# Performance work log

Measured on AMD Instinct MI355X. Metric: run time of the kernel, lower is better.

The kernel has to match this reference:

```python
import jax, jax.numpy as jnp
import numpy as np

N_ACTIVE = 100000
C = 64
N_BLOCKS = 2
K = 27  # 3x3x3 submanifold rulebook offsets
BN_EPS = 1e-4  # scn BatchNorm default eps


def setup_inputs() -> dict:
    key = jax.random.key(0)
    k1, k2, k3 = jax.random.split(key, 3)
    feats = jax.random.normal(k1, (N_ACTIVE, C), dtype=jnp.float32)
    # rulebook: index N_ACTIVE == missing neighbor (points at padded zero row)
    nbrs = jax.random.randint(k2, (N_ACTIVE, K), 0, N_ACTIVE + 1, dtype=jnp.int32)
    # make the center offset (k=13) point at self, as in a real submanifold rulebook
    nbrs = nbrs.at[:, K // 2].set(jnp.arange(N_ACTIVE, dtype=jnp.int32))
    fan_in = K * C
    W = jax.random.normal(k3, (N_BLOCKS, 2, K, C, C), dtype=jnp.float32) / np.sqrt(fan_in)
    gamma = jnp.ones((N_BLOCKS, 2, C), dtype=jnp.float32)
    beta = jnp.zeros((N_BLOCKS, 2, C), dtype=jnp.float32)
    return {"feats": feats, "nbrs": nbrs, "W": W, "gamma": gamma, "beta": beta}


def _subm_conv(x, nbrs, Wk):
    # x: [N, C]; nbrs: [N, K] with value N meaning 'missing'; Wk: [K, C, C]
    x_pad = jnp.concatenate([x, jnp.zeros((1, x.shape[1]), x.dtype)], axis=0)
    g = x_pad[nbrs]  # [N, K, C] rulebook gather
    return jnp.einsum('nkc,kcd->nd', g, Wk)  # gather-GEMM-scatter fused by contraction


def _bn(x, g, b):
    mu = jnp.mean(x, axis=0)
    var = jnp.var(x, axis=0)
    return (x - mu) * jax.lax.rsqrt(var + BN_EPS) * g + b


def reference(feats, nbrs, W, gamma, beta):
    x = feats
    for i in range(N_BLOCKS):  # SparseResidualBlock chain
        residual = x
        out = _subm_conv(x, nbrs, W[i, 0])
        out = jax.nn.relu(_bn(out, gamma[i, 0], beta[i, 0]))  # BatchNormReLU
        out = _subm_conv(out, nbrs, W[i, 1])
        out = _bn(out, gamma[i, 1], beta[i, 1])  # BatchNormalization
        x = jax.nn.relu(out + residual)  # AddTable + ReLU
    return x
```

## Files before the change

### kernel.cpp

```cpp
#include <hip/hip_runtime.h>

#define N_PTS 100000
#define NT_STRIDE 100096
#define NK 27
#define NKP 28
#define TOTAL (N_PTS * 64)
#define NB_CONV 1564

typedef short bf16x8 __attribute__((ext_vector_type(8)));
typedef float f32x4 __attribute__((ext_vector_type(4)));
typedef unsigned short u16x8 __attribute__((ext_vector_type(8)));

__device__ __forceinline__ unsigned short f2bf(float f) {
    unsigned u = __builtin_bit_cast(unsigned, f);
    u += 0x7fffu + ((u >> 16) & 1u);
    return (unsigned short)(u >> 16);
}
__device__ __forceinline__ float bf2f(unsigned short u) {
    return __builtin_bit_cast(float, ((unsigned)u) << 16);
}

__global__ void cast_in_k(const float* __restrict__ feats, unsigned short* __restrict__ xb) {
    int t = blockIdx.x * 256 + threadIdx.x;
    if (t >= (N_PTS + 1) * 8) return;
    int i = t * 8;
    u16x8 o;
    if (i < TOTAL) {
        f32x4 v0 = ((const f32x4*)(feats + i))[0];
        f32x4 v1 = ((const f32x4*)(feats + i))[1];
#pragma unroll
        for (int j = 0; j < 4; ++j) { o[j] = f2bf(v0[j]); o[4 + j] = f2bf(v1[j]); }
    } else {
#pragma unroll
        for (int j = 0; j < 8; ++j) o[j] = 0;
    }
    *(u16x8*)(xb + i) = o;
}

__global__ void tr_nbrs_k(const int* __restrict__ nbrs, int* __restrict__ nbrsT) {
    __shared__ int tile[64 * 28];
    const int n0 = blockIdx.x * 64;
    const int t = threadIdx.x;
    const int base = n0 * 27;
    for (int i = t; i < 1728; i += 256) {
        int v = (base + i < N_PTS * 27) ? nbrs[base + i] : N_PTS;
        int r = i / 27, c = i - r * 27;
        tile[r * 28 + c] = v;
    }
    __syncthreads();
    for (int i = t; i < 1728; i += 256) {
        int k = i >> 6, j = i & 63;
        nbrsT[(size_t)k * NT_STRIDE + n0 + j] = tile[j * 28 + k];
    }
    for (int i = t; i < 64; i += 256)
        nbrsT[(size_t)27 * NT_STRIDE + n0 + i] = N_PTS;
}

__global__ void pack_w_k(const float* __restrict__ W, unsigned short* __restrict__ Wp) {
    int o = blockIdx.x * 256 + threadIdx.x;
    if (o >= 4 * NKP * 4096) return;
    int conv = o / (NKP * 4096);
    int r = o - conv * (NKP * 4096);
    int k = r >> 12;
    if (k == 27) { Wp[o] = 0; return; }
    int r2 = r & 4095;
    int frag = r2 >> 9;
    int kk = frag >> 2, cb = frag & 3;
    int lane = (r2 >> 3) & 63;
    int j = r2 & 7;
    int c = kk * 32 + (lane >> 4) * 8 + j;
    int d = cb * 16 + (lane & 15);
    Wp[o] = f2bf(W[(size_t)(conv * NK + k) * 4096 + c * 64 + d]);
}

__global__ __launch_bounds__(256, 4) void conv_k(
    const unsigned short* __restrict__ xb,
    const int* __restrict__ nbrsT,
    const unsigned short* __restrict__ Wp,
    unsigned short* __restrict__ ybf,
    float* __restrict__ partials)
{
    const int tid = threadIdx.x;
    const int lane = tid & 63;
    const int wave = tid >> 6;
    const int l15 = lane & 15;
    const int lgrp = lane >> 4;
    const int h = wave & 1;
    const int kh = wave >> 1;
    const int wave_row = blockIdx.x * 64 + h * 32;
    const int r0 = wave_row + l15;
    const int r1 = r0 + 16;
    const int k0 = kh * 14;

    f32x4 acc[2][4];
#pragma unroll
    for (int m = 0; m < 2; ++m)
#pragma unroll
        for (int cb = 0; cb < 4; ++cb) acc[m][cb] = (f32x4)0.f;

    const bf16x8* wp = (const bf16x8*)Wp;

    int id0[4], id1[4];
#pragma unroll
    for (int s = 0; s < 4; ++s) {
        id0[s] = nbrsT[(size_t)(k0 + s) * NT_STRIDE + r0];
        id1[s] = nbrsT[(size_t)(k0 + s) * NT_STRIDE + r1];
    }
    bf16x8 apf[3][4];
#pragma unroll
    for (int s = 0; s < 2; ++s) {
        const bf16x8* p0 = (const bf16x8*)(xb + (size_t)id0[s] * 64);
        const bf16x8* p1 = (const bf16x8*)(xb + (size_t)id1[s] * 64);
        apf[s][0] = p0[lgrp]; apf[s][1] = p0[4 + lgrp];
        apf[s][2] = p1[lgrp]; apf[s][3] = p1[4 + lgrp];
    }

#pragma unroll
    for (int s = 0; s < 14; ++s) {
        if (s + 4 < 14) {
            id0[s & 3] = nbrsT[(size_t)(k0 + s + 4) * NT_STRIDE + r0];
            id1[s & 3] = nbrsT[(size_t)(k0 + s + 4) * NT_STRIDE + r1];
        }
        if (s + 2 < 14) {
            const int j = (s + 2) & 3;
            const int st = (s + 2) % 3;
            const bf16x8* p0 = (const bf16x8*)(xb + (size_t)id0[j] * 64);
            const bf16x8* p1 = (const bf16x8*)(xb + (size_t)id1[j] * 64);
            apf[st][0] = p0[lgrp]; apf[st][1] = p0[4 + lgrp];
            apf[st][2] = p1[lgrp]; apf[st][3] = p1[4 + lgrp];
        }
        __builtin_amdgcn_sched_barrier(0);
        const int st = s % 3;
        const bf16x8* wk = wp + (size_t)(k0 + s) * 512 + lane;
        {
            bf16x8 b0 = wk[0], b1 = wk[64], b2 = wk[128], b3 = wk[192];
            acc[0][0] = __builtin_amdgcn_mfma_f32_16x16x32_bf16(apf[st][0], b0, acc[0][0], 0, 0, 0);
            acc[1][0] = __builtin_amdgcn_mfma_f32_16x16x32_bf16(apf[st][2], b0, acc[1][0], 0, 0, 0);
            acc[0][1] = __builtin_amdgcn_mfma_f32_16x16x32_bf16(apf[st][0], b1, acc[0][1], 0, 0, 0);
            acc[1][1] = __builtin_amdgcn_mfma_f32_16x16x32_bf16(apf[st][2], b1, acc[1][1], 0, 0, 0);
            acc[0][2] = __builtin_amdgcn_mfma_f32_16x16x32_bf16(apf[st][0], b2, acc[0][2], 0, 0, 0);
            acc[1][2] = __builtin_amdgcn_mfma_f32_16x16x32_bf16(apf[st][2], b2, acc[1][2], 0, 0, 0);
            acc[0][3] = __builtin_amdgcn_mfma_f32_16x16x32_bf16(apf[st][0], b3, acc[0][3], 0, 0, 0);
            acc[1][3] = __builtin_amdgcn_mfma_f32_16x16x32_bf16(apf[st][2], b3, acc[1][3], 0, 0, 0);
        }
        {
            bf16x8 b0 = wk[256], b1 = wk[320], b2 = wk[384], b3 = wk[448];
            acc[0][0] = __builtin_amdgcn_mfma_f32_16x16x32_bf16(apf[st][1], b0, acc[0][0], 0, 0, 0);
            acc[1][0] = __builtin_amdgcn_mfma_f32_16x16x32_bf16(apf[st][3], b0, acc[1][0], 0, 0, 0);
            acc[0][1] = __builtin_amdgcn_mfma_f32_16x16x32_bf16(apf[st][1], b1, acc[0][1], 0, 0, 0);
            acc[1][1] = __builtin_amdgcn_mfma_f32_16x16x32_bf16(apf[st][3], b1, acc[1][1], 0, 0, 0);
            acc[0][2] = __builtin_amdgcn_mfma_f32_16x16x32_bf16(apf[st][1], b2, acc[0][2], 0, 0, 0);
            acc[1][2] = __builtin_amdgcn_mfma_f32_16x16x32_bf16(apf[st][3], b2, acc[1][2], 0, 0, 0);
            acc[0][3] = __builtin_amdgcn_mfma_f32_16x16x32_bf16(apf[st][1], b3, acc[0][3], 0, 0, 0);
            acc[1][3] = __builtin_amdgcn_mfma_f32_16x16x32_bf16(apf[st][3], b3, acc[1][3], 0, 0, 0);
        }
    }

    __shared__ __align__(16) float ytile[64 * 68];
    __shared__ __align__(16) float sred[4][128];

    if (kh == 0) {
#pragma unroll
        for (int m = 0; m < 2; ++m)
#pragma unroll
            for (int cb = 0; cb < 4; ++cb)
#pragma unroll
                for (int r = 0; r < 4; ++r)
                    ytile[(h * 32 + m * 16 + lgrp * 4 + r) * 68 + cb * 16 + l15] = acc[m][cb][r];
    }
    __syncthreads();
    if (kh == 1) {
#pragma unroll
        for (int m = 0; m < 2; ++m)
#pragma unroll
            for (int cb = 0; cb < 4; ++cb)
#pragma unroll
                for (int r = 0; r < 4; ++r)
                    ytile[(h * 32 + m * 16 + lgrp * 4 + r) * 68 + cb * 16 + l15] += acc[m][cb][r];
    }
    __syncthreads();

    const int row = tid >> 2;
    const int colb = (tid & 3) * 16;
    f32x4 v[4];
#pragma unroll
    for (int j = 0; j < 4; ++j) v[j] = *(const f32x4*)&ytile[row * 68 + colb + 4 * j];

    const int grow = blockIdx.x * 64 + row;
    if (grow < N_PTS) {
        u16x8 o0, o1;
#pragma unroll
        for (int j = 0; j < 4; ++j) { o0[j] = f2bf(v[0][j]); o0[4 + j] = f2bf(v[1][j]); }
#pragma unroll
        for (int j = 0; j < 4; ++j) { o1[j] = f2bf(v[2][j]); o1[4 + j] = f2bf(v[3][j]); }
        *(u16x8*)(ybf + (size_t)grow * 64 + colb) = o0;
        *(u16x8*)(ybf + (size_t)grow * 64 + colb + 8) = o1;
    }

    f32x4 sv[4], s2v[4];
#pragma unroll
    for (int j = 0; j < 4; ++j) { sv[j] = v[j]; s2v[j] = v[j] * v[j]; }
#pragma unroll
    for (int off = 4; off < 64; off <<= 1) {
#pragma unroll
        for (int j = 0; j < 4; ++j) {
#pragma unroll
            for (int e = 0; e < 4; ++e) {
                sv[j][e]  += __shfl_xor(sv[j][e],  off);
                s2v[j][e] += __shfl_xor(s2v[j][e], off);
            }
        }
    }
    if (lane < 4) {
#pragma unroll
        for (int j = 0; j < 4; ++j) {
            *(f32x4*)&sred[wave][lane * 16 + 4 * j]      = sv[j];
            *(f32x4*)&sred[wave][64 + lane * 16 + 4 * j] = s2v[j];
        }
    }
    __syncthreads();
    if (tid < 128) {
        float p = sred[0][tid] + sred[1][tid] + sred[2][tid] + sred[3][tid];
        partials[(size_t)blockIdx.x * 128 + tid] = p;
    }
}

__global__ void bn_fin_k(const float* __restrict__ partials,
                         const float* __restrict__ gamma,
                         const float* __restrict__ beta,
                         float* __restrict__ scsh) {
    const int c = blockIdx.x;
    const int t = threadIdx.x;
    float s = 0.f, s2 = 0.f;
    for (int w = t; w < NB_CONV; w += 256) {
        s  += partials[(size_t)w * 128 + c];
        s2 += partials[(size_t)w * 128 + 64 + c];
    }
#pragma unroll
    for (int off = 1; off < 64; off <<= 1) {
        s  += __shfl_xor(s, off, 64);
        s2 += __shfl_xor(s2, off, 64);
    }
    __shared__ float sm[8];
    int wv = t >> 6;
    if ((t & 63) == 0) { sm[wv] = s; sm[4 + wv] = s2; }
    __syncthreads();
    if (t == 0) {
        float S  = sm[0] + sm[1] + sm[2] + sm[3];
        float S2 = sm[4] + sm[5] + sm[6] + sm[7];
        const float invN = 1.0f / (float)N_PTS;
        float mu = S * invN;
        float var = S2 * invN - mu * mu;
        float sc = gamma[c] * rsqrtf(var + 1e-4f);
        scsh[c] = sc;
        scsh[64 + c] = beta[c] - mu * sc;
    }
}

__global__ void bn_relu_cast_k(const unsigned short* __restrict__ ybf, const float* __restrict__ scsh,
                               unsigned short* __restrict__ xb) {
    int t = blockIdx.x * 256 + threadIdx.x;
    if (t >= TOTAL / 8) return;
    int i = t * 8;
    int c0 = i & 63;
    u16x8 v = *(const u16x8*)(ybf + i);
    f32x4 sa = *(const f32x4*)(scsh + c0);
    f32x4 sb = *(const f32x4*)(scsh + c0 + 4);
    f32x4 ba = *(const f32x4*)(scsh + 64 + c0);
    f32x4 bb = *(const f32x4*)(scsh + 64 + c0 + 4);
    u16x8 o;
#pragma unroll
    for (int j = 0; j < 4; ++j) {
        o[j]     = f2bf(fmaxf(bf2f(v[j])     * sa[j] + ba[j], 0.f));
        o[4 + j] = f2bf(fmaxf(bf2f(v[4 + j]) * sb[j] + bb[j], 0.f));
    }
    *(u16x8*)(xb + i) = o;
}

__global__ void bn_add_relu_k(const unsigned short* __restrict__ ybf, const float* __restrict__ scsh,
                              const float* __restrict__ res, float* __restrict__ xout,
                              unsigned short* __restrict__ xb, int writeBf) {
    int t = blockIdx.x * 256 + threadIdx.x;
    if (t >= TOTAL / 8) return;
    int i = t * 8;
    int c0 = i & 63;
    u16x8 v = *(const u16x8*)(ybf + i);
    f32x4 q0 = ((const f32x4*)(res + i))[0];
    f32x4 q1 = ((const f32x4*)(res + i))[1];
    f32x4 sa = *(const f32x4*)(scsh + c0);
    f32x4 sb = *(const f32x4*)(scsh + c0 + 4);
    f32x4 ba = *(const f32x4*)(scsh + 64 + c0);
    f32x4 bb = *(const f32x4*)(scsh + 64 + c0 + 4);
    f32x4 o0, o1;
#pragma unroll
    for (int j = 0; j < 4; ++j) {
        o0[j] = fmaxf(bf2f(v[j])     * sa[j] + ba[j] + q0[j], 0.f);
        o1[j] = fmaxf(bf2f(v[4 + j]) * sb[j] + bb[j] + q1[j], 0.f);
    }
    ((f32x4*)(xout + i))[0] = o0;
    ((f32x4*)(xout + i))[1] = o1;
    if (writeBf) {
        u16x8 o;
#pragma unroll
        for (int j = 0; j < 4; ++j) { o[j] = f2bf(o0[j]); o[4 + j] = f2bf(o1[j]); }
        *(u16x8*)(xb + i) = o;
    }
}

extern "C" void kernel_launch(void* const* d_in, const int* in_sizes, int n_in,
                              void* d_out, int out_size, void* d_ws, size_t ws_size,
                              hipStream_t stream) {
    const float* feats = (const float*)d_in[0];
    const int*   nbrs  = (const int*)d_in[1];
    const float* W     = (const float*)d_in[2];
    const float* gamma = (const float*)d_in[3];
    const float* beta  = (const float*)d_in[4];
    float* out = (float*)d_out;

    char* ws = (char*)d_ws;
    unsigned short* xb       = (unsigned short*)ws;
    unsigned short* ybf      = (unsigned short*)(ws + 12800512);
    unsigned short* Wp       = (unsigned short*)(ws + 25600512);
    int*            nbrsT    = (int*)(ws + 26518016);
    float*          partials = (float*)(ws + 37728768);
    float*          scsh     = (float*)(ws + 38529536);

    dim3 b256(256);
    cast_in_k<<<((N_PTS + 1) * 8 + 255) / 256, b256, 0, stream>>>(feats, xb);
    tr_nbrs_k<<<NT_STRIDE / 64, b256, 0, stream>>>(nbrs, nbrsT);
    pack_w_k<<<(4 * NKP * 4096) / 256, b256, 0, stream>>>(W, Wp);

    const int appl_blocks = (TOTAL / 8) / 256;
    for (int blk = 0; blk < 2; ++blk) {
        int c0 = blk * 2, c1 = blk * 2 + 1;
        conv_k<<<NB_CONV, b256, 0, stream>>>(xb, nbrsT, Wp + (size_t)c0 * NKP * 4096, ybf, partials);
        bn_fin_k<<<64, b256, 0, stream>>>(partials, gamma + c0 * 64, beta + c0 * 64, scsh);
        bn_relu_cast_k<<<appl_blocks, b256, 0, stream>>>(ybf, scsh, xb);
        conv_k<<<NB_CONV, b256, 0, stream>>>(xb, nbrsT, Wp + (size_t)c1 * NKP * 4096, ybf, partials);
        bn_fin_k<<<64, b256, 0, stream>>>(partials, gamma + c1 * 64, beta + c1 * 64, scsh);
        const float* res = (blk == 0) ? feats : (const float*)out;
        bn_add_relu_k<<<appl_blocks, b256, 0, stream>>>(ybf, scsh, res, out, xb, blk == 0 ? 1 : 0);
    }
}
```

Before: 472.8 us.

## Fuse BN+ReLU into second conv gather and use atomic BN statistics

The first BN+ReLU is now applied on the fly while the second conv gathers neighbour rows, so the separate normalize pass over the intermediate is gone. Missing neighbours are still forced to zero. The per-block partial-sum reduction kernel is replaced by atomicAdd into a small global accumulator that is zeroed once with a memset, and every consumer derives scale and shift itself. The cost is redundant BN math on each gathered row (27x per point), float-atomic contention, nondeterministic summation order, and the removal of a sched_barrier. Nontemporal loads and stores are also added.

```diff
diff --git a/kernel.cpp b/kernel.cpp
--- a/kernel.cpp
+++ b/kernel.cpp
@@ -73,12 +73,16 @@
     Wp[o] = f2bf(W[(size_t)(conv * NK + k) * 4096 + c * 64 + d]);
 }
 
+template <int FUSED>
 __global__ __launch_bounds__(256, 4) void conv_k(
-    const unsigned short* __restrict__ xb,
+    const unsigned short* __restrict__ xin,
     const int* __restrict__ nbrsT,
     const unsigned short* __restrict__ Wp,
-    unsigned short* __restrict__ ybf,
-    float* __restrict__ partials)
+    unsigned short* __restrict__ yout,
+    const float* __restrict__ gpart_in,
+    const float* __restrict__ gamma,
+    const float* __restrict__ beta,
+    float* __restrict__ gpart_out)
 {
     const int tid = threadIdx.x;
     const int lane = tid & 63;
@@ -92,6 +96,25 @@
     const int r1 = r0 + 16;
     const int k0 = kh * 14;
 
+    float sc[2][8], sh[2][8];
+    if (FUSED) {
+        const float invN = 1.0f / (float)N_PTS;
+#pragma unroll
+        for (int half = 0; half < 2; ++half) {
+            int cbase = half * 32 + lgrp * 8;
+#pragma unroll
+            for (int e = 0; e < 8; ++e) {
+                int c = cbase + e;
+                float S = gpart_in[c], S2 = gpart_in[64 + c];
+                float mu = S * invN;
+                float var = S2 * invN - mu * mu;
+                float s = gamma[c] * rsqrtf(var + 1e-4f);
+                sc[half][e] = s;
+                sh[half][e] = beta[c] - mu * s;
+            }
+        }
+    }
+
     f32x4 acc[2][4];
 #pragma unroll
     for (int m = 0; m < 2; ++m)
@@ -100,36 +123,53 @@
 
     const bf16x8* wp = (const bf16x8*)Wp;
 
+    auto ldrow = [&](int idx, bf16x8* dst) {
+        const bf16x8* p = (const bf16x8*)(xin + (size_t)idx * 64);
+        bf16x8 a0 = p[lgrp];
+        bf16x8 a1 = p[4 + lgrp];
+        if (FUSED) {
+            bool ok = (idx != N_PTS);
+            u16x8 u0 = __builtin_bit_cast(u16x8, a0);
+            u16x8 u1 = __builtin_bit_cast(u16x8, a1);
+            u16x8 o0, o1;
+#pragma unroll
+            for (int e = 0; e < 8; ++e) {
+                o0[e] = f2bf(fmaxf(bf2f(u0[e]) * sc[0][e] + sh[0][e], 0.f));
+                o1[e] = f2bf(fmaxf(bf2f(u1[e]) * sc[1][e] + sh[1][e], 0.f));
+            }
+            bf16x8 z = (bf16x8)(short)0;
+            a0 = ok ? __builtin_bit_cast(bf16x8, o0) : z;
+            a1 = ok ? __builtin_bit_cast(bf16x8, o1) : z;
+        }
+        dst[0] = a0;
+        dst[1] = a1;
+    };
+
     int id0[4], id1[4];
 #pragma unroll
     for (int s = 0; s < 4; ++s) {
-        id0[s] = nbrsT[(size_t)(k0 + s) * NT_STRIDE + r0];
-        id1[s] = nbrsT[(size_t)(k0 + s) * NT_STRIDE + r1];
+        id0[s] = __builtin_nontemporal_load(nbrsT + (size_t)(k0 + s) * NT_STRIDE + r0);
+        id1[s] = __builtin_nontemporal_load(nbrsT + (size_t)(k0 + s) * NT_STRIDE + r1);
     }
     bf16x8 apf[3][4];
 #pragma unroll
     for (int s = 0; s < 2; ++s) {
-        const bf16x8* p0 = (const bf16x8*)(xb + (size_t)id0[s] * 64);
-        const bf16x8* p1 = (const bf16x8*)(xb + (size_t)id1[s] * 64);
-        apf[s][0] = p0[lgrp]; apf[s][1] = p0[4 + lgrp];
-        apf[s][2] = p1[lgrp]; apf[s][3] = p1[4 + lgrp];
+        ldrow(id0[s], &apf[s][0]);
+        ldrow(id1[s], &apf[s][2]);
     }
 
 #pragma unroll
     for (int s = 0; s < 14; ++s) {
         if (s + 4 < 14) {
-            id0[s & 3] = nbrsT[(size_t)(k0 + s + 4) * NT_STRIDE + r0];
-            id1[s & 3] = nbrsT[(size_t)(k0 + s + 4) * NT_STRIDE + r1];
+            id0[s & 3] = __builtin_nontemporal_load(nbrsT + (size_t)(k0 + s + 4) * NT_STRIDE + r0);
+            id1[s & 3] = __builtin_nontemporal_load(nbrsT + (size_t)(k0 + s + 4) * NT_STRIDE + r1);
         }
         if (s + 2 < 14) {
             const int j = (s + 2) & 3;
-            const int st = (s + 2) % 3;
-            const bf16x8* p0 = (const bf16x8*)(xb + (size_t)id0[j] * 64);
-            const bf16x8* p1 = (const bf16x8*)(xb + (size_t)id1[j] * 64);
-            apf[st][0] = p0[lgrp]; apf[st][1] = p0[4 + lgrp];
-            apf[st][2] = p1[lgrp]; apf[st][3] = p1[4 + lgrp];
-        }
-        __builtin_amdgcn_sched_barrier(0);
+            const int st2 = (s + 2) % 3;
+            ldrow(id0[j], &apf[st2][0]);
+            ldrow(id1[j], &apf[st2][2]);
+        }
         const int st = s % 3;
         const bf16x8* wk = wp + (size_t)(k0 + s) * 512 + lane;
         {
@@ -193,8 +233,8 @@
         for (int j = 0; j < 4; ++j) { o0[j] = f2bf(v[0][j]); o0[4 + j] = f2bf(v[1][j]); }
 #pragma unroll
         for (int j = 0; j < 4; ++j) { o1[j] = f2bf(v[2][j]); o1[4 + j] = f2bf(v[3][j]); }
-        *(u16x8*)(ybf + (size_t)grow * 64 + colb) = o0;
-        *(u16x8*)(ybf + (size_t)grow * 64 + colb + 8) = o1;
+        __builtin_nontemporal_store(o0, (u16x8*)(yout + (size_t)grow * 64 + colb));
+        __builtin_nontemporal_store(o1, (u16x8*)(yout + (size_t)grow * 64 + colb + 8));
     }
 
     f32x4 sv[4], s2v[4];
@@ -221,84 +261,45 @@
     __syncthreads();
     if (tid < 128) {
         float p = sred[0][tid] + sred[1][tid] + sred[2][tid] + sred[3][tid];
-        partials[(size_t)blockIdx.x * 128 + tid] = p;
-    }
-}
-
-__global__ void bn_fin_k(const float* __restrict__ partials,
-                         const float* __restrict__ gamma,
-                         const float* __restrict__ beta,
-                         float* __restrict__ scsh) {
-    const int c = blockIdx.x;
-    const int t = threadIdx.x;
-    float s = 0.f, s2 = 0.f;
-    for (int w = t; w < NB_CONV; w += 256) {
-        s  += partials[(size_t)w * 128 + c];
-        s2 += partials[(size_t)w * 128 + 64 + c];
-    }
-#pragma unroll
-    for (int off = 1; off < 64; off <<= 1) {
-        s  += __shfl_xor(s, off, 64);
-        s2 += __shfl_xor(s2, off, 64);
-    }
-    __shared__ float sm[8];
-    int wv = t >> 6;
-    if ((t & 63) == 0) { sm[wv] = s; sm[4 + wv] = s2; }
-    __syncthreads();
-    if (t == 0) {
-        float S  = sm[0] + sm[1] + sm[2] + sm[3];
-        float S2 = sm[4] + sm[5] + sm[6] + sm[7];
-        const float invN = 1.0f / (float)N_PTS;
-        float mu = S * invN;
-        float var = S2 * invN - mu * mu;
-        float sc = gamma[c] * rsqrtf(var + 1e-4f);
-        scsh[c] = sc;
-        scsh[64 + c] = beta[c] - mu * sc;
-    }
-}
-
-__global__ void bn_relu_cast_k(const unsigned short* __restrict__ ybf, const float* __restrict__ scsh,
-                               unsigned short* __restrict__ xb) {
+        atomicAdd(&gpart_out[tid], p);
+    }
+}
+
+__global__ void bn_fuse_k(const unsigned short* __restrict__ yraw,
+                          const float* __restrict__ gpart,
+                          const float* __restrict__ gamma,
+                          const float* __restrict__ beta,
+                          const float* __restrict__ res,
+                          float* __restrict__ xout,
+                          unsigned short* __restrict__ xb, int writeBf) {
     int t = blockIdx.x * 256 + threadIdx.x;
     if (t >= TOTAL / 8) return;
     int i = t * 8;
     int c0 = i & 63;
-    u16x8 v = *(const u16x8*)(ybf + i);
-    f32x4 sa = *(const f32x4*)(scsh + c0);
-    f32x4 sb = *(const f32x4*)(scsh + c0 + 4);
-    f32x4 ba = *(const f32x4*)(scsh + 64 + c0);
-    f32x4 bb = *(const f32x4*)(scsh + 64 + c0 + 4);
-    u16x8 o;
+    u16x8 v = __builtin_nontemporal_load((const u16x8*)(yraw + i));
+    f32x4 q0 = __builtin_nontemporal_load((const f32x4*)(res + i));
+    f32x4 q1 = __builtin_nontemporal_load((const f32x4*)(res + i) + 1);
+
+    const float invN = 1.0f / (float)N_PTS;
+    float sc[8], sh[8];
+#pragma unroll
+    for (int j = 0; j < 8; ++j) {
+        int c = c0 + j;
+        float S = gpart[c], S2 = gpart[64 + c];
+        float mu = S * invN;
+        float var = S2 * invN - mu * mu;
+        float s = gamma[c] * rsqrtf(var + 1e-4f);
+        sc[j] = s;
+        sh[j] = beta[c] - mu * s;
+    }
+    f32x4 o0, o1;
 #pragma unroll
     for (int j = 0; j < 4; ++j) {
-        o[j]     = f2bf(fmaxf(bf2f(v[j])     * sa[j] + ba[j], 0.f));
-        o[4 + j] = f2bf(fmaxf(bf2f(v[4 + j]) * sb[j] + bb[j], 0.f));
-    }
-    *(u16x8*)(xb + i) = o;
-}
-
-__global__ void bn_add_relu_k(const unsigned short* __restrict__ ybf, const float* __restrict__ scsh,
-                              const float* __restrict__ res, float* __restrict__ xout,
-                              unsigned short* __restrict__ xb, int writeBf) {
-    int t = blockIdx.x * 256 + threadIdx.x;
-    if (t >= TOTAL / 8) return;
-    int i = t * 8;
-    int c0 = i & 63;
-    u16x8 v = *(const u16x8*)(ybf + i);
-    f32x4 q0 = ((const f32x4*)(res + i))[0];
-    f32x4 q1 = ((const f32x4*)(res + i))[1];
-    f32x4 sa = *(const f32x4*)(scsh + c0);
-    f32x4 sb = *(const f32x4*)(scsh + c0 + 4);
-    f32x4 ba = *(const f32x4*)(scsh + 64 + c0);
-    f32x4 bb = *(const f32x4*)(scsh + 64 + c0 + 4);
-    f32x4 o0, o1;
-#pragma unroll
-    for (int j = 0; j < 4; ++j) {
-        o0[j] = fmaxf(bf2f(v[j])     * sa[j] + ba[j] + q0[j], 0.f);
-        o1[j] = fmaxf(bf2f(v[4 + j]) * sb[j] + bb[j] + q1[j], 0.f);
-    }
-    ((f32x4*)(xout + i))[0] = o0;
-    ((f32x4*)(xout + i))[1] = o1;
+        o0[j] = fmaxf(bf2f(v[j])     * sc[j]     + sh[j]     + q0[j], 0.f);
+        o1[j] = fmaxf(bf2f(v[4 + j]) * sc[4 + j] + sh[4 + j] + q1[j], 0.f);
+    }
+    __builtin_nontemporal_store(o0, (f32x4*)(xout + i));
+    __builtin_nontemporal_store(o1, (f32x4*)(xout + i) + 1);
     if (writeBf) {
         u16x8 o;
 #pragma unroll
@@ -318,27 +319,29 @@
     float* out = (float*)d_out;
 
     char* ws = (char*)d_ws;
-    unsigned short* xb       = (unsigned short*)ws;
-    unsigned short* ybf      = (unsigned short*)(ws + 12800512);
-    unsigned short* Wp       = (unsigned short*)(ws + 25600512);
-    int*            nbrsT    = (int*)(ws + 26518016);
-    float*          partials = (float*)(ws + 37728768);
-    float*          scsh     = (float*)(ws + 38529536);
+    unsigned short* xb    = (unsigned short*)ws;
+    unsigned short* ybf   = (unsigned short*)(ws + 12800512);
+    unsigned short* Wp    = (unsigned short*)(ws + 25601024);
+    int*            nbrsT = (int*)(ws + 26518528);
+    float*          gpart = (float*)(ws + 37729280);
 
     dim3 b256(256);
+    hipMemsetAsync(gpart, 0, 4 * 128 * sizeof(float), stream);
     cast_in_k<<<((N_PTS + 1) * 8 + 255) / 256, b256, 0, stream>>>(feats, xb);
     tr_nbrs_k<<<NT_STRIDE / 64, b256, 0, stream>>>(nbrs, nbrsT);
     pack_w_k<<<(4 * NKP * 4096) / 256, b256, 0, stream>>>(W, Wp);
 
     const int appl_blocks = (TOTAL / 8) / 256;
     for (int blk = 0; blk < 2; ++blk) {
-        int c0 = blk * 2, c1 = blk * 2 + 1;
-        conv_k<<<NB_CONV, b256, 0, stream>>>(xb, nbrsT, Wp + (size_t)c0 * NKP * 4096, ybf, partials);
-        bn_fin_k<<<64, b256, 0, stream>>>(partials, gamma + c0 * 64, beta + c0 * 64, scsh);
-        bn_relu_cast_k<<<appl_blocks, b256, 0, stream>>>(ybf, scsh, xb);
-        conv_k<<<NB_CONV, b256, 0, stream>>>(xb, nbrsT, Wp + (size_t)c1 * NKP * 4096, ybf, partials);
-        bn_fin_k<<<64, b256, 0, stream>>>(partials, gamma + c1 * 64, beta + c1 * 64, scsh);
-        const float* res = (blk == 0) ? feats : (const float*)out;
-        bn_add_relu_k<<<appl_blocks, b256, 0, stream>>>(ybf, scsh, res, out, xb, blk == 0 ? 1 : 0);
-    }
-}
+        const int c0 = blk * 2, c1 = blk * 2 + 1;
+        conv_k<0><<<NB_CONV, b256, 0, stream>>>(
+            xb, nbrsT, Wp + (size_t)c0 * NKP * 4096, ybf,
+            nullptr, nullptr, nullptr, gpart + c0 * 128);
+        conv_k<1><<<NB_CONV, b256, 0, stream>>>(
+            ybf, nbrsT, Wp + (size_t)c1 * NKP * 4096, xb,
+            gpart + c0 * 128, gamma + c0 * 64, beta + c0 * 64, gpart + c1 * 128);
+        const float* resp = (blk == 0) ? feats : (const float*)out;
+        bn_fuse_k<<<appl_blocks, b256, 0, stream>>>(
+            xb, gpart + c1 * 128, gamma + c1 * 64, beta + c1 * 64, resp, out, xb, blk == 0 ? 1 : 0);
+    }
+}
```

Measured after the change: 592.7 us. 1.25x slower.
